# Performance work log

Hardware: AMD Instinct MI355X
Metric: run time of the kernel (lower is better)

Reference implementation:

```python
import jax, jax.numpy as jnp
import numpy as np

T, K = 2048, 6          # tokens, activated experts per token
DIM = 2048              # model dim
INTER = 1408            # moe intermediate dim
E = 16                  # routed experts (group_size, shared not fused)


def setup_inputs() -> dict:
    key = jax.random.key(0)
    k1, k2, k3, k4, k5, k6 = jax.random.split(key, 6)
    x = jax.random.normal(k1, (T, DIM), dtype=jnp.float32)
    weights = jax.random.uniform(k2, (T, K), dtype=jnp.float32)
    indices = jax.random.randint(k3, (T, K), 0, E, dtype=jnp.int64)
    s = 1.0 / np.sqrt(DIM)
    Wg = jax.random.normal(k4, (E, INTER, DIM), dtype=jnp.float32) * s
    Wu = jax.random.normal(k5, (E, INTER, DIM), dtype=jnp.float32) * s
    Wd = jax.random.normal(k6, (E, DIM, INTER), dtype=jnp.float32) * (1.0 / np.sqrt(INTER))
    return {"x": x, "weights": weights, "indices": indices,
            "Wg": Wg, "Wu": Wu, "Wd": Wd}


def reference(x, weights, indices, Wg, Wu, Wd):
    # per-token combine weight for each expert: [T, E]
    # gate_w[t, e] = sum_k weights[t, k] * (indices[t, k] == e)
    one_hot = jax.nn.one_hot(indices, E, dtype=x.dtype)        # [T, K, E]
    gate_w = jnp.einsum('tk,tke->te', weights, one_hot)        # [T, E]

    # SwiGLU expert FFN, dense over experts, combine folded pre-down-proj
    g = jnp.einsum('td,eid->tei', x, Wg)                       # [T, E, INTER]
    u = jnp.einsum('td,eid->tei', x, Wu)                       # [T, E, INTER]
    act = jax.nn.silu(g) * u                                   # [T, E, INTER]
    # y[t] = sum_e gate_w[t,e] * (act[t,e] @ Wd[e].T)
    y = jnp.einsum('tei,edi->td', act * gate_w[:, :, None], Wd)  # [T, DIM]
    return y
```

## Files before the change

### kernel.cpp

```cpp
#include <hip/hip_runtime.h>
#include <hip/hip_bf16.h>
#include <cstdint>

#define TT     2048
#define KSEL   6
#define DMODEL 2048
#define DINTER 1408
#define NE     16
#define PMAX   (TT * KSEL)

typedef short bf16x8 __attribute__((ext_vector_type(8)));
typedef float f32x4 __attribute__((ext_vector_type(4)));
typedef unsigned short u16;
typedef u16 u16x8 __attribute__((ext_vector_type(8)));

__device__ __forceinline__ u16 f2bf(float f) {
  union { float f; unsigned u; } v; v.f = f;
  return (u16)((v.u + 0x7FFFu + ((v.u >> 16) & 1u)) >> 16);
}

__device__ __forceinline__ void gl2lds16(const void* g, void* l) {
  __builtin_amdgcn_global_load_lds((const __attribute__((address_space(1))) void*)g,
                                   (__attribute__((address_space(3))) void*)l,
                                   16, 0, 0);
}

__global__ void k_gate(const float* __restrict__ w, const int* __restrict__ idx,
                       float* __restrict__ gate_w, int* __restrict__ counts) {
  int g = blockIdx.x * 256 + threadIdx.x;
  int t = g >> 4, e = g & 15;
  const int* ip = idx + t * KSEL;
  const float* wp = w + t * KSEL;
  float s = 0.f;
#pragma unroll
  for (int k = 0; k < KSEL; ++k) s += (ip[k] == e) ? wp[k] : 0.f;
  gate_w[g] = s;
  if (s != 0.f) atomicAdd(counts + e, 1);
}

__global__ void k_scan(const int* __restrict__ counts, int* __restrict__ offs) {
  if (threadIdx.x == 0 && blockIdx.x == 0) {
    int r = 0;
#pragma unroll
    for (int e = 0; e < NE; ++e) { offs[e] = r; r += counts[e]; }
    offs[NE] = r;
  }
}

__global__ void k_fill(const float* __restrict__ gate_w, const int* __restrict__ offs,
                       int* __restrict__ cursor, int* __restrict__ slot_tok,
                       float* __restrict__ slot_gate) {
  int g = blockIdx.x * 256 + threadIdx.x;
  int t = g >> 4, e = g & 15;
  float s = gate_w[g];
  if (s != 0.f) {
    int p = atomicAdd(cursor + e, 1);
    int sl = offs[e] + p;
    slot_tok[sl] = t;
    slot_gate[sl] = s;
  }
}

__global__ void k_castw(const float* __restrict__ src, u16* __restrict__ dst, int n8) {
  int stride = gridDim.x * 256;
  for (int i = blockIdx.x * 256 + threadIdx.x; i < n8; i += stride) {
    const float4* p = (const float4*)src + (size_t)i * 2;
    float4 v0 = p[0], v1 = p[1];
    u16x8 o;
    o[0] = f2bf(v0.x); o[1] = f2bf(v0.y); o[2] = f2bf(v0.z); o[3] = f2bf(v0.w);
    o[4] = f2bf(v1.x); o[5] = f2bf(v1.y); o[6] = f2bf(v1.z); o[7] = f2bf(v1.w);
    *(u16x8*)(dst + (size_t)i * 8) = o;
  }
}

__global__ __launch_bounds__(256, 2) void k_gemm1(
    const u16* __restrict__ xb, const u16* __restrict__ wgb, const u16* __restrict__ wub,
    const int* __restrict__ slot_tok, const float* __restrict__ slot_gate,
    const int* __restrict__ offs, const int* __restrict__ counts,
    u16* __restrict__ act) {
  int b = blockIdx.x;
  int w = (b & 7) * 352 + (b >> 3);
  int mt = w & 15, rest = w >> 4;
  int it = rest % 11, e = rest / 11;

  int mcount = counts[e];
  if (mt * 128 >= mcount) return;
  int mrem = mcount - mt * 128; if (mrem > 128) mrem = 128;
  int slotBase = offs[e] + mt * 128;
  int iBase = it * 128;

  __shared__ u16 sA[128 * 64];
  __shared__ u16 sG[128 * 64];
  __shared__ u16 sU[128 * 64];
  __shared__ int tokLds[128];
  __shared__ float gateLds[128];

  int tid = threadIdx.x;
  if (tid < 128) {
    int rl = tid < mrem ? tid : 0;
    tokLds[tid] = slot_tok[slotBase + rl];
    gateLds[tid] = (tid < mrem) ? slot_gate[slotBase + rl] : 0.f;
  }
  __syncthreads();

  int wv = tid >> 6, lane = tid & 63;
  const u16 *aSrc[4], *gSrc[4], *uSrc[4];
  u16 *aDst[4], *gDst[4], *uDst[4];
  const u16* gBase = wgb + ((size_t)e * DINTER + iBase) * DMODEL;
  const u16* uBase = wub + ((size_t)e * DINTER + iBase) * DMODEL;
#pragma unroll
  for (int i2 = 0; i2 < 4; ++i2) {
    int chunk = wv * 4 + i2;
    int row = chunk * 8 + (lane >> 3);
    int colOff = (lane & 7) * 8;
    aSrc[i2] = xb + (size_t)tokLds[row] * DMODEL + colOff;
    gSrc[i2] = gBase + (size_t)row * DMODEL + colOff;
    uSrc[i2] = uBase + (size_t)row * DMODEL + colOff;
    aDst[i2] = sA + chunk * 512;
    gDst[i2] = sG + chunk * 512;
    uDst[i2] = sU + chunk * 512;
  }

  f32x4 accg[4][4] = {};
  f32x4 accu[4][4] = {};
  int fr = lane & 15, fq = lane >> 4;
  int wr = (wv >> 1) * 64, wc = (wv & 1) * 64;

  for (int kb = 0; kb < DMODEL / 64; ++kb) {
    int kOff = kb * 64;
    __syncthreads();
#pragma unroll
    for (int i2 = 0; i2 < 4; ++i2) {
      gl2lds16(aSrc[i2] + kOff, aDst[i2]);
      gl2lds16(gSrc[i2] + kOff, gDst[i2]);
      gl2lds16(uSrc[i2] + kOff, uDst[i2]);
    }
    __syncthreads();
#pragma unroll
    for (int kf = 0; kf < 2; ++kf) {
      bf16x8 af[4], bg[4], bu[4];
#pragma unroll
      for (int mf = 0; mf < 4; ++mf)
        af[mf] = *(const bf16x8*)&sA[(wr + mf * 16 + fr) * 64 + kf * 32 + fq * 8];
#pragma unroll
      for (int nf = 0; nf < 4; ++nf) {
        bg[nf] = *(const bf16x8*)&sG[(wc + nf * 16 + fr) * 64 + kf * 32 + fq * 8];
        bu[nf] = *(const bf16x8*)&sU[(wc + nf * 16 + fr) * 64 + kf * 32 + fq * 8];
      }
#pragma unroll
      for (int mf = 0; mf < 4; ++mf)
#pragma unroll
        for (int nf = 0; nf < 4; ++nf) {
          accg[mf][nf] = __builtin_amdgcn_mfma_f32_16x16x32_bf16(af[mf], bg[nf], accg[mf][nf], 0, 0, 0);
          accu[mf][nf] = __builtin_amdgcn_mfma_f32_16x16x32_bf16(af[mf], bu[nf], accu[mf][nf], 0, 0, 0);
        }
    }
  }
#pragma unroll
  for (int mf = 0; mf < 4; ++mf)
#pragma unroll
    for (int nf = 0; nf < 4; ++nf)
#pragma unroll
      for (int r = 0; r < 4; ++r) {
        int row = wr + mf * 16 + fq * 4 + r;
        if (row < mrem) {
          float g = accg[mf][nf][r], u = accu[mf][nf][r];
          float a = g / (1.f + __expf(-g)) * u * gateLds[row];
          act[(size_t)(slotBase + row) * DINTER + iBase + wc + nf * 16 + fr] = f2bf(a);
        }
      }
}

__global__ __launch_bounds__(256, 4) void k_gemm2(
    const u16* __restrict__ act, const u16* __restrict__ wdb,
    const int* __restrict__ slot_tok, const int* __restrict__ offs,
    const int* __restrict__ counts, float* __restrict__ y) {
  int b = blockIdx.x;
  int w = (b & 7) * 512 + (b >> 3);
  int mt = w & 15, rest = w >> 4;
  int dt = rest & 15, e = rest >> 4;

  int mcount = counts[e];
  if (mt * 128 >= mcount) return;
  int mrem = mcount - mt * 128; if (mrem > 128) mrem = 128;
  int slotBase = offs[e] + mt * 128;
  int dBase = dt * 128;

  __shared__ u16 sA[128 * 64];
  __shared__ u16 sB[128 * 64];
  __shared__ int tokLds[128];

  int tid = threadIdx.x;
  if (tid < 128) tokLds[tid] = slot_tok[slotBase + (tid < mrem ? tid : 0)];
  __syncthreads();

  int wv = tid >> 6, lane = tid & 63;
  const u16 *aSrc[4], *bSrc[4];
  u16 *aDst[4], *bDst[4];
  const u16* bBase = wdb + ((size_t)e * DMODEL + dBase) * DINTER;
#pragma unroll
  for (int i2 = 0; i2 < 4; ++i2) {
    int chunk = wv * 4 + i2;
    int row = chunk * 8 + (lane >> 3);
    int colOff = (lane & 7) * 8;
    aSrc[i2] = act + (size_t)(slotBase + row) * DINTER + colOff;
    bSrc[i2] = bBase + (size_t)row * DINTER + colOff;
    aDst[i2] = sA + chunk * 512;
    bDst[i2] = sB + chunk * 512;
  }

  f32x4 acc[4][4] = {};
  int fr = lane & 15, fq = lane >> 4;
  int wr = (wv >> 1) * 64, wc = (wv & 1) * 64;

  for (int kb = 0; kb < DINTER / 64; ++kb) {
    int kOff = kb * 64;
    __syncthreads();
#pragma unroll
    for (int i2 = 0; i2 < 4; ++i2) {
      gl2lds16(aSrc[i2] + kOff, aDst[i2]);
      gl2lds16(bSrc[i2] + kOff, bDst[i2]);
    }
    __syncthreads();
#pragma unroll
    for (int kf = 0; kf < 2; ++kf) {
      bf16x8 af[4], bb[4];
#pragma unroll
      for (int mf = 0; mf < 4; ++mf)
        af[mf] = *(const bf16x8*)&sA[(wr + mf * 16 + fr) * 64 + kf * 32 + fq * 8];
#pragma unroll
      for (int nf = 0; nf < 4; ++nf)
        bb[nf] = *(const bf16x8*)&sB[(wc + nf * 16 + fr) * 64 + kf * 32 + fq * 8];
#pragma unroll
      for (int mf = 0; mf < 4; ++mf)
#pragma unroll
        for (int nf = 0; nf < 4; ++nf)
          acc[mf][nf] = __builtin_amdgcn_mfma_f32_16x16x32_bf16(af[mf], bb[nf], acc[mf][nf], 0, 0, 0);
    }
  }
#pragma unroll
  for (int mf = 0; mf < 4; ++mf)
#pragma unroll
    for (int nf = 0; nf < 4; ++nf)
#pragma unroll
      for (int r = 0; r < 4; ++r) {
        int row = wr + mf * 16 + fq * 4 + r;
        if (row < mrem) {
          int t = tokLds[row];
          atomicAdd(y + (size_t)t * DMODEL + dBase + wc + nf * 16 + fr, acc[mf][nf][r]);
        }
      }
}

extern "C" void kernel_launch(void* const* d_in, const int* in_sizes, int n_in,
                              void* d_out, int out_size, void* d_ws, size_t ws_size,
                              hipStream_t stream) {
  const float* x       = (const float*)d_in[0];
  const float* weights = (const float*)d_in[1];
  const int*   indices = (const int*)d_in[2];
  const float* Wg      = (const float*)d_in[3];
  const float* Wu      = (const float*)d_in[4];
  const float* Wd      = (const float*)d_in[5];
  float* y = (float*)d_out;

  const size_t WELEM = (size_t)NE * DINTER * DMODEL;

  char* ws = (char*)d_ws;
  size_t o = 0;
  float* gate_w = (float*)(ws + o); o += (size_t)TT * NE * 4;
  size_t ctrlOff = o;
  int* counts = (int*)(ws + o);
  int* offs   = (int*)(ws + o + 64);
  int* cursor = (int*)(ws + o + 192);
  o += 256;
  int*   slot_tok  = (int*)(ws + o);   o += (size_t)PMAX * 4;
  float* slot_gate = (float*)(ws + o); o += (size_t)PMAX * 4;
  u16* xb  = (u16*)(ws + o); o += (size_t)TT * DMODEL * 2;
  u16* act = (u16*)(ws + o); o += (size_t)(PMAX + 128) * DINTER * 2;
  u16* wgb = (u16*)(ws + o); o += WELEM * 2;
  u16* wub = (u16*)(ws + o); o += WELEM * 2;
  u16* wdb = (u16*)(ws + o); o += WELEM * 2;
  (void)ws_size; (void)in_sizes; (void)n_in;

  hipMemsetAsync(d_out, 0, (size_t)out_size * 4, stream);
  hipMemsetAsync(ws + ctrlOff, 0, 256, stream);

  k_gate<<<TT * NE / 256, 256, 0, stream>>>(weights, indices, gate_w, counts);
  k_scan<<<1, 64, 0, stream>>>(counts, offs);
  k_fill<<<TT * NE / 256, 256, 0, stream>>>(gate_w, offs, cursor, slot_tok, slot_gate);
  k_castw<<<(TT * DMODEL / 8) / 256, 256, 0, stream>>>(x, xb, TT * DMODEL / 8);
  k_castw<<<2048, 256, 0, stream>>>(Wg, wgb, (int)(WELEM / 8));
  k_castw<<<2048, 256, 0, stream>>>(Wu, wub, (int)(WELEM / 8));
  k_castw<<<2048, 256, 0, stream>>>(Wd, wdb, (int)(WELEM / 8));
  k_gemm1<<<2816, 256, 0, stream>>>(xb, wgb, wub, slot_tok, slot_gate, offs, counts, act);
  k_gemm2<<<4096, 256, 0, stream>>>(act, wdb, slot_tok, offs, counts, y);
}
```

Baseline: 632.3 us.

## Double-buffer LDS tiles and enlarge M tile to 256 in both MoE GEMMs

Both grouped GEMM kernels now run 512 threads per block with a 256-row token tile, so each weight tile loaded into LDS is reused across twice as many tokens. The K loop is double-buffered: the next tile is issued with global_load_lds while MFMAs run on the current buffer, using a single vmcnt(0) wait plus barrier per step. MFMA sections are wrapped in s_setprio. The cost is much larger LDS use (about 128KB for gemm1), which likely allows only one block per CU, and more wasted work on partially filled tiles for experts whose token count is not a multiple of 256.

```diff
diff --git a/kernel.cpp b/kernel.cpp
--- a/kernel.cpp
+++ b/kernel.cpp
@@ -24,6 +24,11 @@
                                    (__attribute__((address_space(3))) void*)l,
                                    16, 0, 0);
 }
+
+#define VMCNT0_BAR() do { \
+  asm volatile("s_waitcnt vmcnt(0)" ::: "memory"); \
+  __builtin_amdgcn_s_barrier(); \
+} while (0)
 
 __global__ void k_gate(const float* __restrict__ w, const int* __restrict__ idx,
                        float* __restrict__ gate_w, int* __restrict__ counts) {
@@ -73,30 +78,30 @@
   }
 }
 
-__global__ __launch_bounds__(256, 2) void k_gemm1(
+__global__ __launch_bounds__(512, 2) void k_gemm1(
     const u16* __restrict__ xb, const u16* __restrict__ wgb, const u16* __restrict__ wub,
     const int* __restrict__ slot_tok, const float* __restrict__ slot_gate,
     const int* __restrict__ offs, const int* __restrict__ counts,
     u16* __restrict__ act) {
   int b = blockIdx.x;
-  int w = (b & 7) * 352 + (b >> 3);
-  int mt = w & 15, rest = w >> 4;
+  int w = (b & 7) * 176 + (b >> 3);
+  int mt = w & 7, rest = w >> 3;
   int it = rest % 11, e = rest / 11;
 
   int mcount = counts[e];
-  if (mt * 128 >= mcount) return;
-  int mrem = mcount - mt * 128; if (mrem > 128) mrem = 128;
-  int slotBase = offs[e] + mt * 128;
+  if (mt * 256 >= mcount) return;
+  int mrem = mcount - mt * 256; if (mrem > 256) mrem = 256;
+  int slotBase = offs[e] + mt * 256;
   int iBase = it * 128;
 
-  __shared__ u16 sA[128 * 64];
-  __shared__ u16 sG[128 * 64];
-  __shared__ u16 sU[128 * 64];
-  __shared__ int tokLds[128];
-  __shared__ float gateLds[128];
+  __shared__ u16 sA[2][256 * 64];
+  __shared__ u16 sG[2][128 * 64];
+  __shared__ u16 sU[2][128 * 64];
+  __shared__ int tokLds[256];
+  __shared__ float gateLds[256];
 
   int tid = threadIdx.x;
-  if (tid < 128) {
+  if (tid < 256) {
     int rl = tid < mrem ? tid : 0;
     tokLds[tid] = slot_tok[slotBase + rl];
     gateLds[tid] = (tid < mrem) ? slot_gate[slotBase + rl] : 0.f;
@@ -104,21 +109,26 @@
   __syncthreads();
 
   int wv = tid >> 6, lane = tid & 63;
-  const u16 *aSrc[4], *gSrc[4], *uSrc[4];
-  u16 *aDst[4], *gDst[4], *uDst[4];
+  const u16 *aSrc[4], *gSrc[2], *uSrc[2];
+  int aOff[4], gOff[2], uOff[2];
   const u16* gBase = wgb + ((size_t)e * DINTER + iBase) * DMODEL;
   const u16* uBase = wub + ((size_t)e * DINTER + iBase) * DMODEL;
+  int colOff = (lane & 7) * 8;
 #pragma unroll
   for (int i2 = 0; i2 < 4; ++i2) {
     int chunk = wv * 4 + i2;
     int row = chunk * 8 + (lane >> 3);
-    int colOff = (lane & 7) * 8;
     aSrc[i2] = xb + (size_t)tokLds[row] * DMODEL + colOff;
+    aOff[i2] = chunk * 512;
+  }
+#pragma unroll
+  for (int i2 = 0; i2 < 2; ++i2) {
+    int chunk = wv * 2 + i2;
+    int row = chunk * 8 + (lane >> 3);
     gSrc[i2] = gBase + (size_t)row * DMODEL + colOff;
     uSrc[i2] = uBase + (size_t)row * DMODEL + colOff;
-    aDst[i2] = sA + chunk * 512;
-    gDst[i2] = sG + chunk * 512;
-    uDst[i2] = sU + chunk * 512;
+    gOff[i2] = chunk * 512;
+    uOff[i2] = chunk * 512;
   }
 
   f32x4 accg[4][4] = {};
@@ -126,27 +136,28 @@
   int fr = lane & 15, fq = lane >> 4;
   int wr = (wv >> 1) * 64, wc = (wv & 1) * 64;
 
-  for (int kb = 0; kb < DMODEL / 64; ++kb) {
-    int kOff = kb * 64;
-    __syncthreads();
-#pragma unroll
-    for (int i2 = 0; i2 < 4; ++i2) {
-      gl2lds16(aSrc[i2] + kOff, aDst[i2]);
-      gl2lds16(gSrc[i2] + kOff, gDst[i2]);
-      gl2lds16(uSrc[i2] + kOff, uDst[i2]);
+  auto STAGE = [&](int buf, int kOff) {
+#pragma unroll
+    for (int i2 = 0; i2 < 4; ++i2) gl2lds16(aSrc[i2] + kOff, &sA[buf][aOff[i2]]);
+#pragma unroll
+    for (int i2 = 0; i2 < 2; ++i2) {
+      gl2lds16(gSrc[i2] + kOff, &sG[buf][gOff[i2]]);
+      gl2lds16(uSrc[i2] + kOff, &sU[buf][uOff[i2]]);
     }
-    __syncthreads();
+  };
+  auto COMPUTE = [&](int buf) {
 #pragma unroll
     for (int kf = 0; kf < 2; ++kf) {
       bf16x8 af[4], bg[4], bu[4];
 #pragma unroll
       for (int mf = 0; mf < 4; ++mf)
-        af[mf] = *(const bf16x8*)&sA[(wr + mf * 16 + fr) * 64 + kf * 32 + fq * 8];
+        af[mf] = *(const bf16x8*)&sA[buf][(wr + mf * 16 + fr) * 64 + kf * 32 + fq * 8];
 #pragma unroll
       for (int nf = 0; nf < 4; ++nf) {
-        bg[nf] = *(const bf16x8*)&sG[(wc + nf * 16 + fr) * 64 + kf * 32 + fq * 8];
-        bu[nf] = *(const bf16x8*)&sU[(wc + nf * 16 + fr) * 64 + kf * 32 + fq * 8];
+        bg[nf] = *(const bf16x8*)&sG[buf][(wc + nf * 16 + fr) * 64 + kf * 32 + fq * 8];
+        bu[nf] = *(const bf16x8*)&sU[buf][(wc + nf * 16 + fr) * 64 + kf * 32 + fq * 8];
       }
+      __builtin_amdgcn_s_setprio(1);
 #pragma unroll
       for (int mf = 0; mf < 4; ++mf)
 #pragma unroll
@@ -154,8 +165,21 @@
           accg[mf][nf] = __builtin_amdgcn_mfma_f32_16x16x32_bf16(af[mf], bg[nf], accg[mf][nf], 0, 0, 0);
           accu[mf][nf] = __builtin_amdgcn_mfma_f32_16x16x32_bf16(af[mf], bu[nf], accu[mf][nf], 0, 0, 0);
         }
+      __builtin_amdgcn_s_setprio(0);
     }
-  }
+  };
+
+  STAGE(0, 0);
+  VMCNT0_BAR();
+  int cur = 0;
+  for (int kb = 0; kb < DMODEL / 64 - 1; ++kb) {
+    STAGE(cur ^ 1, (kb + 1) * 64);
+    COMPUTE(cur);
+    VMCNT0_BAR();
+    cur ^= 1;
+  }
+  COMPUTE(cur);
+
 #pragma unroll
   for (int mf = 0; mf < 4; ++mf)
 #pragma unroll
@@ -171,73 +195,90 @@
       }
 }
 
-__global__ __launch_bounds__(256, 4) void k_gemm2(
+__global__ __launch_bounds__(512, 2) void k_gemm2(
     const u16* __restrict__ act, const u16* __restrict__ wdb,
     const int* __restrict__ slot_tok, const int* __restrict__ offs,
     const int* __restrict__ counts, float* __restrict__ y) {
   int b = blockIdx.x;
-  int w = (b & 7) * 512 + (b >> 3);
-  int mt = w & 15, rest = w >> 4;
+  int w = (b & 7) * 256 + (b >> 3);
+  int mt = w & 7, rest = w >> 3;
   int dt = rest & 15, e = rest >> 4;
 
   int mcount = counts[e];
-  if (mt * 128 >= mcount) return;
-  int mrem = mcount - mt * 128; if (mrem > 128) mrem = 128;
-  int slotBase = offs[e] + mt * 128;
+  if (mt * 256 >= mcount) return;
+  int mrem = mcount - mt * 256; if (mrem > 256) mrem = 256;
+  int slotBase = offs[e] + mt * 256;
   int dBase = dt * 128;
 
-  __shared__ u16 sA[128 * 64];
-  __shared__ u16 sB[128 * 64];
-  __shared__ int tokLds[128];
+  __shared__ u16 sA[2][256 * 64];
+  __shared__ u16 sB[2][128 * 64];
+  __shared__ int tokLds[256];
 
   int tid = threadIdx.x;
-  if (tid < 128) tokLds[tid] = slot_tok[slotBase + (tid < mrem ? tid : 0)];
+  if (tid < 256) tokLds[tid] = slot_tok[slotBase + (tid < mrem ? tid : 0)];
   __syncthreads();
 
   int wv = tid >> 6, lane = tid & 63;
-  const u16 *aSrc[4], *bSrc[4];
-  u16 *aDst[4], *bDst[4];
+  const u16 *aSrc[4], *bSrc[2];
+  int aOff[4], bOff[2];
   const u16* bBase = wdb + ((size_t)e * DMODEL + dBase) * DINTER;
+  int colOff = (lane & 7) * 8;
 #pragma unroll
   for (int i2 = 0; i2 < 4; ++i2) {
     int chunk = wv * 4 + i2;
     int row = chunk * 8 + (lane >> 3);
-    int colOff = (lane & 7) * 8;
     aSrc[i2] = act + (size_t)(slotBase + row) * DINTER + colOff;
+    aOff[i2] = chunk * 512;
+  }
+#pragma unroll
+  for (int i2 = 0; i2 < 2; ++i2) {
+    int chunk = wv * 2 + i2;
+    int row = chunk * 8 + (lane >> 3);
     bSrc[i2] = bBase + (size_t)row * DINTER + colOff;
-    aDst[i2] = sA + chunk * 512;
-    bDst[i2] = sB + chunk * 512;
+    bOff[i2] = chunk * 512;
   }
 
   f32x4 acc[4][4] = {};
   int fr = lane & 15, fq = lane >> 4;
   int wr = (wv >> 1) * 64, wc = (wv & 1) * 64;
 
-  for (int kb = 0; kb < DINTER / 64; ++kb) {
-    int kOff = kb * 64;
-    __syncthreads();
-#pragma unroll
-    for (int i2 = 0; i2 < 4; ++i2) {
-      gl2lds16(aSrc[i2] + kOff, aDst[i2]);
-      gl2lds16(bSrc[i2] + kOff, bDst[i2]);
-    }
-    __syncthreads();
+  auto STAGE = [&](int buf, int kOff) {
+#pragma unroll
+    for (int i2 = 0; i2 < 4; ++i2) gl2lds16(aSrc[i2] + kOff, &sA[buf][aOff[i2]]);
+#pragma unroll
+    for (int i2 = 0; i2 < 2; ++i2) gl2lds16(bSrc[i2] + kOff, &sB[buf][bOff[i2]]);
+  };
+  auto COMPUTE = [&](int buf) {
 #pragma unroll
     for (int kf = 0; kf < 2; ++kf) {
       bf16x8 af[4], bb[4];
 #pragma unroll
       for (int mf = 0; mf < 4; ++mf)
-        af[mf] = *(const bf16x8*)&sA[(wr + mf * 16 + fr) * 64 + kf * 32 + fq * 8];
+        af[mf] = *(const bf16x8*)&sA[buf][(wr + mf * 16 + fr) * 64 + kf * 32 + fq * 8];
 #pragma unroll
       for (int nf = 0; nf < 4; ++nf)
-        bb[nf] = *(const bf16x8*)&sB[(wc + nf * 16 + fr) * 64 + kf * 32 + fq * 8];
+        bb[nf] = *(const bf16x8*)&sB[buf][(wc + nf * 16 + fr) * 64 + kf * 32 + fq * 8];
+      __builtin_amdgcn_s_setprio(1);
 #pragma unroll
       for (int mf = 0; mf < 4; ++mf)
 #pragma unroll
         for (int nf = 0; nf < 4; ++nf)
           acc[mf][nf] = __builtin_amdgcn_mfma_f32_16x16x32_bf16(af[mf], bb[nf], acc[mf][nf], 0, 0, 0);
+      __builtin_amdgcn_s_setprio(0);
     }
-  }
+  };
+
+  STAGE(0, 0);
+  VMCNT0_BAR();
+  int cur = 0;
+  for (int kb = 0; kb < DINTER / 64 - 1; ++kb) {
+    STAGE(cur ^ 1, (kb + 1) * 64);
+    COMPUTE(cur);
+    VMCNT0_BAR();
+    cur ^= 1;
+  }
+  COMPUTE(cur);
+
 #pragma unroll
   for (int mf = 0; mf < 4; ++mf)
 #pragma unroll
@@ -276,7 +317,7 @@
   int*   slot_tok  = (int*)(ws + o);   o += (size_t)PMAX * 4;
   float* slot_gate = (float*)(ws + o); o += (size_t)PMAX * 4;
   u16* xb  = (u16*)(ws + o); o += (size_t)TT * DMODEL * 2;
-  u16* act = (u16*)(ws + o); o += (size_t)(PMAX + 128) * DINTER * 2;
+  u16* act = (u16*)(ws + o); o += (size_t)(PMAX + 256) * DINTER * 2;
   u16* wgb = (u16*)(ws + o); o += WELEM * 2;
   u16* wub = (u16*)(ws + o); o += WELEM * 2;
   u16* wdb = (u16*)(ws + o); o += WELEM * 2;
@@ -292,6 +333,6 @@
   k_castw<<<2048, 256, 0, stream>>>(Wg, wgb, (int)(WELEM / 8));
   k_castw<<<2048, 256, 0, stream>>>(Wu, wub, (int)(WELEM / 8));
   k_castw<<<2048, 256, 0, stream>>>(Wd, wdb, (int)(WELEM / 8));
-  k_gemm1<<<2816, 256, 0, stream>>>(xb, wgb, wub, slot_tok, slot_gate, offs, counts, act);
-  k_gemm2<<<4096, 256, 0, stream>>>(act, wdb, slot_tok, offs, counts, y);
-}
+  k_gemm1<<<1408, 512, 0, stream>>>(xb, wgb, wub, slot_tok, slot_gate, offs, counts, act);
+  k_gemm2<<<2048, 512, 0, stream>>>(act, wdb, slot_tok, offs, counts, y);
+}
```

Measured after the change: 738.7 us. 1.17x slower.

## XOR-swizzle LDS tiles in both GEMMs and merge cast kernels into one launch

Applied to the files above, without the earlier changes.

Both expert GEMMs now store their 64-column bf16 LDS tiles with an XOR swizzle on the 16-byte chunk index (chunk ^ row&7). The global-to-LDS load source column and the fragment read offsets are permuted to match, which is meant to remove LDS bank conflicts on the MFMA fragment reads. Separately, the four fp32-to-bf16 cast launches for x and the three weight tensors are merged into one grid-stride kernel that picks its source per index, saving three launches. The merged cast adds a branch per element, and the swizzle depends on the load and read permutations agreeing.

```diff
diff --git a/kernel.cpp b/kernel.cpp
--- a/kernel.cpp
+++ b/kernel.cpp
@@ -61,17 +61,29 @@
   }
 }
 
-__global__ void k_castw(const float* __restrict__ src, u16* __restrict__ dst, int n8) {
+#define XV8   (TT * DMODEL / 8)
+#define WV8   (NE * DINTER * DMODEL / 8)
+__global__ void k_castall(const float* __restrict__ x,  u16* __restrict__ xb,
+                          const float* __restrict__ wg, u16* __restrict__ wgb,
+                          const float* __restrict__ wu, u16* __restrict__ wub,
+                          const float* __restrict__ wd, u16* __restrict__ wdb) {
+  const int total = XV8 + 3 * WV8;
   int stride = gridDim.x * 256;
-  for (int i = blockIdx.x * 256 + threadIdx.x; i < n8; i += stride) {
-    const float4* p = (const float4*)src + (size_t)i * 2;
+  for (int i = blockIdx.x * 256 + threadIdx.x; i < total; i += stride) {
+    const float* src; u16* dst; int j;
+    if (i < XV8)                { src = x;  dst = xb;  j = i; }
+    else if (i < XV8 + WV8)     { src = wg; dst = wgb; j = i - XV8; }
+    else if (i < XV8 + 2 * WV8) { src = wu; dst = wub; j = i - XV8 - WV8; }
+    else                        { src = wd; dst = wdb; j = i - XV8 - 2 * WV8; }
+    const float4* p = (const float4*)src + (size_t)j * 2;
     float4 v0 = p[0], v1 = p[1];
     u16x8 o;
     o[0] = f2bf(v0.x); o[1] = f2bf(v0.y); o[2] = f2bf(v0.z); o[3] = f2bf(v0.w);
     o[4] = f2bf(v1.x); o[5] = f2bf(v1.y); o[6] = f2bf(v1.z); o[7] = f2bf(v1.w);
-    *(u16x8*)(dst + (size_t)i * 8) = o;
-  }
-}
+    *(u16x8*)(dst + (size_t)j * 8) = o;
+  }
+}
+
 
 __global__ __launch_bounds__(256, 2) void k_gemm1(
     const u16* __restrict__ xb, const u16* __restrict__ wgb, const u16* __restrict__ wub,
@@ -108,11 +120,12 @@
   u16 *aDst[4], *gDst[4], *uDst[4];
   const u16* gBase = wgb + ((size_t)e * DINTER + iBase) * DMODEL;
   const u16* uBase = wub + ((size_t)e * DINTER + iBase) * DMODEL;
+  int r8 = lane >> 3;
+  int colOff = (((lane & 7) ^ r8)) * 8;
 #pragma unroll
   for (int i2 = 0; i2 < 4; ++i2) {
     int chunk = wv * 4 + i2;
-    int row = chunk * 8 + (lane >> 3);
-    int colOff = (lane & 7) * 8;
+    int row = chunk * 8 + r8;
     aSrc[i2] = xb + (size_t)tokLds[row] * DMODEL + colOff;
     gSrc[i2] = gBase + (size_t)row * DMODEL + colOff;
     uSrc[i2] = uBase + (size_t)row * DMODEL + colOff;
@@ -140,12 +153,17 @@
     for (int kf = 0; kf < 2; ++kf) {
       bf16x8 af[4], bg[4], bu[4];
 #pragma unroll
-      for (int mf = 0; mf < 4; ++mf)
-        af[mf] = *(const bf16x8*)&sA[(wr + mf * 16 + fr) * 64 + kf * 32 + fq * 8];
+      for (int mf = 0; mf < 4; ++mf) {
+        int row = wr + mf * 16 + fr;
+        int cu = ((kf * 4 + fq) ^ (row & 7)) * 8;
+        af[mf] = *(const bf16x8*)&sA[row * 64 + cu];
+      }
 #pragma unroll
       for (int nf = 0; nf < 4; ++nf) {
-        bg[nf] = *(const bf16x8*)&sG[(wc + nf * 16 + fr) * 64 + kf * 32 + fq * 8];
-        bu[nf] = *(const bf16x8*)&sU[(wc + nf * 16 + fr) * 64 + kf * 32 + fq * 8];
+        int row = wc + nf * 16 + fr;
+        int cu = ((kf * 4 + fq) ^ (row & 7)) * 8;
+        bg[nf] = *(const bf16x8*)&sG[row * 64 + cu];
+        bu[nf] = *(const bf16x8*)&sU[row * 64 + cu];
       }
 #pragma unroll
       for (int mf = 0; mf < 4; ++mf)
@@ -198,11 +216,12 @@
   const u16 *aSrc[4], *bSrc[4];
   u16 *aDst[4], *bDst[4];
   const u16* bBase = wdb + ((size_t)e * DMODEL + dBase) * DINTER;
+  int r8 = lane >> 3;
+  int colOff = (((lane & 7) ^ r8)) * 8;
 #pragma unroll
   for (int i2 = 0; i2 < 4; ++i2) {
     int chunk = wv * 4 + i2;
-    int row = chunk * 8 + (lane >> 3);
-    int colOff = (lane & 7) * 8;
+    int row = chunk * 8 + r8;
     aSrc[i2] = act + (size_t)(slotBase + row) * DINTER + colOff;
     bSrc[i2] = bBase + (size_t)row * DINTER + colOff;
     aDst[i2] = sA + chunk * 512;
@@ -226,11 +245,17 @@
     for (int kf = 0; kf < 2; ++kf) {
       bf16x8 af[4], bb[4];
 #pragma unroll
-      for (int mf = 0; mf < 4; ++mf)
-        af[mf] = *(const bf16x8*)&sA[(wr + mf * 16 + fr) * 64 + kf * 32 + fq * 8];
-#pragma unroll
-      for (int nf = 0; nf < 4; ++nf)
-        bb[nf] = *(const bf16x8*)&sB[(wc + nf * 16 + fr) * 64 + kf * 32 + fq * 8];
+      for (int mf = 0; mf < 4; ++mf) {
+        int row = wr + mf * 16 + fr;
+        int cu = ((kf * 4 + fq) ^ (row & 7)) * 8;
+        af[mf] = *(const bf16x8*)&sA[row * 64 + cu];
+      }
+#pragma unroll
+      for (int nf = 0; nf < 4; ++nf) {
+        int row = wc + nf * 16 + fr;
+        int cu = ((kf * 4 + fq) ^ (row & 7)) * 8;
+        bb[nf] = *(const bf16x8*)&sB[row * 64 + cu];
+      }
 #pragma unroll
       for (int mf = 0; mf < 4; ++mf)
 #pragma unroll
@@ -288,10 +313,7 @@
   k_gate<<<TT * NE / 256, 256, 0, stream>>>(weights, indices, gate_w, counts);
   k_scan<<<1, 64, 0, stream>>>(counts, offs);
   k_fill<<<TT * NE / 256, 256, 0, stream>>>(gate_w, offs, cursor, slot_tok, slot_gate);
-  k_castw<<<(TT * DMODEL / 8) / 256, 256, 0, stream>>>(x, xb, TT * DMODEL / 8);
-  k_castw<<<2048, 256, 0, stream>>>(Wg, wgb, (int)(WELEM / 8));
-  k_castw<<<2048, 256, 0, stream>>>(Wu, wub, (int)(WELEM / 8));
-  k_castw<<<2048, 256, 0, stream>>>(Wd, wdb, (int)(WELEM / 8));
+  k_castall<<<2048, 256, 0, stream>>>(x, xb, Wg, wgb, Wu, wub, Wd, wdb);
   k_gemm1<<<2816, 256, 0, stream>>>(xb, wgb, wub, slot_tok, slot_gate, offs, counts, act);
   k_gemm2<<<4096, 256, 0, stream>>>(act, wdb, slot_tok, offs, counts, y);
 }
```

Measured after the change: 592.1 us. 6.3% less time.
